# Kernel tuning notes

Hardware: AMD Instinct MI355X
Metric: run time of the kernel (lower is better)

## Reference

```python
import jax, jax.numpy as jnp
import numpy as np

N = 8192          # total proposals
D_IN = 256 * 7 * 7  # 12544
HID = 1024
C = 3


def setup_inputs() -> dict:
    key = jax.random.key(0)
    ks = jax.random.split(key, 9)
    s_in = 1.0 / np.sqrt(D_IN)
    s_h = 1.0 / np.sqrt(HID)
    return {
        "feature_vectors": jax.random.normal(ks[0], (N, D_IN), dtype=jnp.float32),
        "W1": jax.random.uniform(ks[1], (D_IN, HID), jnp.float32, -s_in, s_in),
        "b1": jax.random.uniform(ks[2], (HID,), jnp.float32, -s_in, s_in),
        "W2": jax.random.uniform(ks[3], (HID, HID), jnp.float32, -s_h, s_h),
        "b2": jax.random.uniform(ks[4], (HID,), jnp.float32, -s_h, s_h),
        "Wc": jax.random.uniform(ks[5], (HID, C + 1), jnp.float32, -s_h, s_h),
        "bc": jax.random.uniform(ks[6], (C + 1,), jnp.float32, -s_h, s_h),
        "Wr": jax.random.uniform(ks[7], (HID, 4 * C), jnp.float32, -s_h, s_h),
        "br": jax.random.uniform(ks[8], (4 * C,), jnp.float32, -s_h, s_h),
    }


def reference(feature_vectors, W1, b1, W2, b2, Wc, bc, Wr, br):
    # intermediate: Linear -> Linear -> ReLU (note: no ReLU between the two Linears,
    # matching the original nn.Sequential ordering)
    h = feature_vectors @ W1 + b1          # [N, 1024]
    h = h @ W2 + b2                        # [N, 1024]
    h = jax.nn.relu(h)
    class_logits = jax.nn.softmax(h @ Wc + bc, axis=-1)  # [N, C+1]
    box_pred = h @ Wr + br                  # [N, 4C]
    return class_logits, box_pred
```

## Files before the change

### kernel.cpp

```cpp
#include <hip/hip_runtime.h>
#include <hip/hip_bf16.h>
#include <stdint.h>

using u16 = unsigned short;
using u32 = unsigned int;

typedef __attribute__((ext_vector_type(8))) short short8;
typedef __attribute__((ext_vector_type(4))) float floatx4;

__device__ __forceinline__ u16 f2bf(float f) {
  __hip_bfloat16 h = __float2bfloat16(f);
  return *reinterpret_cast<u16*>(&h);
}

__device__ __forceinline__ void gl_lds16(const void* g, void* l) {
  __builtin_amdgcn_global_load_lds((const __attribute__((address_space(1))) void*)g,
                                   (__attribute__((address_space(3))) void*)l, 16, 0, 0);
}

__global__ __launch_bounds__(256)
void transpose_to_bf16(const float* __restrict__ in, u16* __restrict__ out,
                       int R, int Cc) {
  __shared__ float tile[32][33];
  int c0 = blockIdx.x * 32;
  int r0 = blockIdx.y * 32;
  int tx = threadIdx.x;
  int ty = threadIdx.y;
#pragma unroll
  for (int i = 0; i < 32; i += 8)
    tile[ty + i][tx] = in[(size_t)(r0 + ty + i) * Cc + c0 + tx];
  __syncthreads();
#pragma unroll
  for (int i = 0; i < 32; i += 8)
    out[(size_t)(c0 + ty + i) * R + r0 + tx] = f2bf(tile[tx][ty + i]);
}

#define MM(i, j, va, vb) \
  acc[i][j] = __builtin_amdgcn_mfma_f32_16x16x32_bf16(va, vb, acc[i][j], 0, 0, 0)
#define MEMF() asm volatile("" ::: "memory")
#define BAR() do { MEMF(); __builtin_amdgcn_s_barrier(); MEMF(); } while (0)

constexpr int A_BUF  = 256 * 64;
constexpr int B_BUF  = 128 * 64;
constexpr int B_BASE = 3 * A_BUF;
constexpr int LDS_BYTES = (3 * A_BUF + 3 * B_BUF) * 2;

#define STAGE_AH(h, bufo) \
  do { gl_lds16(apt[h][0], lds + (bufo) + adst[h][0]); apt[h][0] += 64; \
       gl_lds16(apt[h][1], lds + (bufo) + adst[h][1]); apt[h][1] += 64; } while (0)
#define STAGE_BH(h, bufo) \
  do { gl_lds16(bpt[h], lds + (bufo) + bdst[h]); bpt[h] += 64; } while (0)

template <bool RELU>
__global__ __launch_bounds__(512, 2)
void gemm256(const u16* __restrict__ A, const u16* __restrict__ BT,
             const float* __restrict__ bias, u16* __restrict__ C,
             int N, int K) {
  extern __shared__ u16 lds[];
  const int tid  = threadIdx.x;
  const int lane = tid & 63;
  const int wave = tid >> 6;
  const int wm = wave >> 1;
  const int wn = wave & 1;
  const int row = lane & 15;
  const int kq  = lane >> 4;
  const int sw  = lane & 7;

  const int orig = blockIdx.y * 8 + blockIdx.x;
  const int rr = ((orig & 7) << 5) | (orig >> 3);
  const int n0 = (rr & 7) * 128;
  const int m0 = (rr >> 3) * 256;

  const int o0 = ((kq) ^ sw) * 8;
  const int o1 = ((4 | kq) ^ sw) * 8;
  const int ar0 = (wm * 64 + row) * 64;
  const int ar1 = ar0 + 16 * 64;
  const int ar2 = ar0 + 32 * 64;
  const int ar3 = ar0 + 48 * 64;
  const int br0 = (wn * 64 + row) * 64;
  const int br1 = br0 + 16 * 64;
  const int br2 = br0 + 32 * 64;
  const int br3 = br0 + 48 * 64;

  const u16* apt[2][2];
  int adst[2][2];
#pragma unroll
  for (int h = 0; h < 2; ++h)
#pragma unroll
    for (int L = 0; L < 2; ++L) {
      int i = L * 512 + tid;
      int rg = h * 128 + (i >> 3);
      int c = i & 7;
      apt[h][L] = A + (size_t)(m0 + rg) * K + ((c ^ (rg & 7)) * 8);
      adst[h][L] = h * 8192 + L * 4096 + wave * 512;
    }
  const u16* bpt[2];
  int bdst[2];
#pragma unroll
  for (int h = 0; h < 2; ++h) {
    int rg = h * 64 + (tid >> 3);
    int c = tid & 7;
    bpt[h] = BT + (size_t)(n0 + rg) * K + ((c ^ (rg & 7)) * 8);
    bdst[h] = B_BASE + h * 4096 + wave * 512;
  }

  STAGE_AH(0, 0);      STAGE_AH(1, 0);      STAGE_BH(0, 0);     STAGE_BH(1, 0);
  STAGE_AH(0, A_BUF);  STAGE_AH(1, A_BUF);  STAGE_BH(0, B_BUF); STAGE_BH(1, B_BUF);
  asm volatile("s_waitcnt vmcnt(6)" ::: "memory");
  BAR();

  floatx4 acc[4][4] = {};
  int cb = 0, sb = 2;
  const int NT = K >> 6;
  for (int T = 0; T < NT; ++T) {
    const bool st = (T + 2 < NT);
    const u16* Ac = lds + cb * A_BUF;
    const u16* Bc = lds + B_BASE + cb * B_BUF;
    const int sA = sb * A_BUF;
    const int sB = sb * B_BUF;

    short8 a0k0, a0k1, a1k0, a1k1, a2k0, a2k1, a3k0, a3k1;
    short8 b0k0, b0k1, b1k0, b1k1, b2k0, b2k1, b3k0, b3k1;

    a0k0 = *(const short8*)(Ac + ar0 + o0);
    a0k1 = *(const short8*)(Ac + ar0 + o1);
    a1k0 = *(const short8*)(Ac + ar1 + o0);
    a1k1 = *(const short8*)(Ac + ar1 + o1);
    b0k0 = *(const short8*)(Bc + br0 + o0);
    b0k1 = *(const short8*)(Bc + br0 + o1);
    b1k0 = *(const short8*)(Bc + br1 + o0);
    b1k1 = *(const short8*)(Bc + br1 + o1);
    if (st) STAGE_AH(0, sA);
    BAR();
    __builtin_amdgcn_s_setprio(1);
    MM(0, 0, a0k0, b0k0); MM(0, 1, a0k0, b1k0);
    MM(1, 0, a1k0, b0k0); MM(1, 1, a1k0, b1k0);
    MM(0, 0, a0k1, b0k1); MM(0, 1, a0k1, b1k1);
    MM(1, 0, a1k1, b0k1); MM(1, 1, a1k1, b1k1);
    __builtin_amdgcn_s_setprio(0);
    BAR();

    b2k0 = *(const short8*)(Bc + br2 + o0);
    b2k1 = *(const short8*)(Bc + br2 + o1);
    b3k0 = *(const short8*)(Bc + br3 + o0);
    b3k1 = *(const short8*)(Bc + br3 + o1);
    if (st) STAGE_AH(1, sA);
    BAR();
    __builtin_amdgcn_s_setprio(1);
    MM(0, 2, a0k0, b2k0); MM(0, 3, a0k0, b3k0);
    MM(1, 2, a1k0, b2k0); MM(1, 3, a1k0, b3k0);
    MM(0, 2, a0k1, b2k1); MM(0, 3, a0k1, b3k1);
    MM(1, 2, a1k1, b2k1); MM(1, 3, a1k1, b3k1);
    __builtin_amdgcn_s_setprio(0);
    BAR();

    a2k0 = *(const short8*)(Ac + ar2 + o0);
    a2k1 = *(const short8*)(Ac + ar2 + o1);
    a3k0 = *(const short8*)(Ac + ar3 + o0);
    a3k1 = *(const short8*)(Ac + ar3 + o1);
    if (st) STAGE_BH(0, sB);
    BAR();
    __builtin_amdgcn_s_setprio(1);
    MM(2, 2, a2k0, b2k0); MM(2, 3, a2k0, b3k0);
    MM(3, 2, a3k0, b2k0); MM(3, 3, a3k0, b3k0);
    MM(2, 2, a2k1, b2k1); MM(2, 3, a2k1, b3k1);
    MM(3, 2, a3k1, b2k1); MM(3, 3, a3k1, b3k1);
    __builtin_amdgcn_s_setprio(0);
    BAR();

    if (st) STAGE_BH(1, sB);
    BAR();
    __builtin_amdgcn_s_setprio(1);
    MM(2, 0, a2k0, b0k0); MM(2, 1, a2k0, b1k0);
    MM(3, 0, a3k0, b0k0); MM(3, 1, a3k0, b1k0);
    MM(2, 0, a2k1, b0k1); MM(2, 1, a2k1, b1k1);
    MM(3, 0, a3k1, b0k1); MM(3, 1, a3k1, b1k1);
    __builtin_amdgcn_s_setprio(0);
    if (st) asm volatile("s_waitcnt vmcnt(6)" ::: "memory");
    else    asm volatile("s_waitcnt vmcnt(0)" ::: "memory");
    BAR();

    cb = (cb == 2) ? 0 : cb + 1;
    sb = (sb == 2) ? 0 : sb + 1;
  }

#pragma unroll
  for (int mt = 0; mt < 4; ++mt) {
#pragma unroll
    for (int nt = 0; nt < 4; ++nt) {
      int gm = m0 + wm * 64 + mt * 16 + kq * 4;
      int gn = n0 + wn * 64 + nt * 16 + row;
      float bv = bias[gn];
#pragma unroll
      for (int r = 0; r < 4; ++r) {
        float v = acc[mt][nt][r] + bv;
        if (RELU) v = fmaxf(v, 0.f);
        C[(size_t)(gm + r) * N + gn] = f2bf(v);
      }
    }
  }
}

constexpr int FA_BUF  = 256 * 64;
constexpr int FB_BUF  = 128 * 64;
constexpr int FB_BASE = 2 * FA_BUF;
constexpr int LDS_BYTES_F = (2 * FA_BUF + 2 * FB_BUF) * 2;

__device__ __forceinline__ void cvtw64(u16* dst, float4 v) {
  u32 lo = (u32)f2bf(v.x) | ((u32)f2bf(v.y) << 16);
  u32 hi = (u32)f2bf(v.z) | ((u32)f2bf(v.w) << 16);
  *(uint2*)dst = make_uint2(lo, hi);
}

__global__ __launch_bounds__(512, 2)
void gemm256F(const float* __restrict__ A, const u16* __restrict__ BT,
              const float* __restrict__ bias, u16* __restrict__ C,
              int N, int K) {
  extern __shared__ u16 lds[];
  const int tid  = threadIdx.x;
  const int lane = tid & 63;
  const int wave = tid >> 6;
  const int wm = wave >> 1;
  const int wn = wave & 1;
  const int row = lane & 15;
  const int kq  = lane >> 4;
  const int sw  = lane & 7;

  const int orig = blockIdx.y * 8 + blockIdx.x;
  const int rr = ((orig & 7) << 5) | (orig >> 3);
  const int n0 = (rr & 7) * 128;
  const int m0 = (rr >> 3) * 256;

  const int o0 = ((kq) ^ sw) * 8;
  const int o1 = ((4 | kq) ^ sw) * 8;
  const int ar0 = (wm * 64 + row) * 64;
  const int ar1 = ar0 + 16 * 64;
  const int ar2 = ar0 + 32 * 64;
  const int ar3 = ar0 + 48 * 64;
  const int br0 = (wn * 64 + row) * 64;
  const int br1 = br0 + 16 * 64;
  const int br2 = br0 + 32 * 64;
  const int br3 = br0 + 48 * 64;

  const u16* bpt[2];
  int bdst[2];
#pragma unroll
  for (int h = 0; h < 2; ++h) {
    int rg = h * 64 + (tid >> 3);
    int c = tid & 7;
    bpt[h] = BT + (size_t)(n0 + rg) * K + ((c ^ (rg & 7)) * 8);
    bdst[h] = h * 4096 + wave * 512;
  }

  const float* aFk = A + (size_t)(m0 + (tid >> 4)) * K + (tid & 15) * 4;
  const int r0t = tid >> 4;
  const int c4 = tid & 15;
  const int adst0 = r0t * 64 + (((c4 >> 1) ^ (r0t & 7)) * 8) + (c4 & 1) * 4;

  float4 rA[2][4];

#define FSTAGE_ISSUE(nB_)                                              \
  do {                                                                 \
    MEMF();                                                            \
    gl_lds16(bpt[0], lds + (nB_) + bdst[0]); bpt[0] += 64;             \
    gl_lds16(bpt[1], lds + (nB_) + bdst[1]); bpt[1] += 64;             \
    MEMF();                                                            \
    _Pragma("unroll")                                                  \
    for (int h = 0; h < 2; ++h)                                        \
      _Pragma("unroll")                                                \
      for (int i = 0; i < 4; ++i)                                      \
        rA[h][i] = *(const float4*)(aFk + (size_t)(h * 128 + i * 32) * K); \
    aFk += 64;                                                         \
    MEMF();                                                            \
  } while (0)

#define FSTAGE_WRITE(nA_)                                              \
  do {                                                                 \
    asm volatile("s_waitcnt vmcnt(4)" ::: "memory");                   \
    _Pragma("unroll")                                                  \
    for (int i = 0; i < 4; ++i)                                        \
      cvtw64(lds + (nA_) + adst0 + (i * 32) * 64, rA[0][i]);           \
    asm volatile("s_waitcnt vmcnt(0)" ::: "memory");                   \
    _Pragma("unroll")                                                  \
    for (int i = 0; i < 4; ++i)                                        \
      cvtw64(lds + (nA_) + adst0 + ((128 + i * 32)) * 64, rA[1][i]);   \
  } while (0)

  FSTAGE_ISSUE(FB_BASE + 0);
  FSTAGE_WRITE(0);
  asm volatile("s_waitcnt lgkmcnt(0)" ::: "memory");
  BAR();

  floatx4 acc[4][4] = {};
  const int NT = K >> 6;
  for (int T = 0; T < NT; ++T) {
    const int cur = T & 1;
    const bool st = (T + 1 < NT);
    const u16* Ac = lds + cur * FA_BUF;
    const u16* Bc = lds + FB_BASE + cur * FB_BUF;
    const int nA = (cur ^ 1) * FA_BUF;
    const int nB = FB_BASE + (cur ^ 1) * FB_BUF;

    short8 a0k0, a0k1, a1k0, a1k1, a2k0, a2k1, a3k0, a3k1;
    short8 b0k0, b0k1, b1k0, b1k1, b2k0, b2k1, b3k0, b3k1;

    a0k0 = *(const short8*)(Ac + ar0 + o0);
    a0k1 = *(const short8*)(Ac + ar0 + o1);
    a1k0 = *(const short8*)(Ac + ar1 + o0);
    a1k1 = *(const short8*)(Ac + ar1 + o1);
    b0k0 = *(const short8*)(Bc + br0 + o0);
    b0k1 = *(const short8*)(Bc + br0 + o1);
    b1k0 = *(const short8*)(Bc + br1 + o0);
    b1k1 = *(const short8*)(Bc + br1 + o1);
    if (st) FSTAGE_ISSUE(nB);
    BAR();
    __builtin_amdgcn_s_setprio(1);
    MM(0, 0, a0k0, b0k0); MM(0, 1, a0k0, b1k0);
    MM(1, 0, a1k0, b0k0); MM(1, 1, a1k0, b1k0);
    MM(0, 0, a0k1, b0k1); MM(0, 1, a0k1, b1k1);
    MM(1, 0, a1k1, b0k1); MM(1, 1, a1k1, b1k1);
    __builtin_amdgcn_s_setprio(0);
    BAR();

    b2k0 = *(const short8*)(Bc + br2 + o0);
    b2k1 = *(const short8*)(Bc + br2 + o1);
    b3k0 = *(const short8*)(Bc + br3 + o0);
    b3k1 = *(const short8*)(Bc + br3 + o1);
    BAR();
    __builtin_amdgcn_s_setprio(1);
    MM(0, 2, a0k0, b2k0); MM(0, 3, a0k0, b3k0);
    MM(1, 2, a1k0, b2k0); MM(1, 3, a1k0, b3k0);
    MM(0, 2, a0k1, b2k1); MM(0, 3, a0k1, b3k1);
    MM(1, 2, a1k1, b2k1); MM(1, 3, a1k1, b3k1);
    __builtin_amdgcn_s_setprio(0);
    BAR();

    a2k0 = *(const short8*)(Ac + ar2 + o0);
    a2k1 = *(const short8*)(Ac + ar2 + o1);
    a3k0 = *(const short8*)(Ac + ar3 + o0);
    a3k1 = *(const short8*)(Ac + ar3 + o1);
    BAR();
    __builtin_amdgcn_s_setprio(1);
    MM(2, 2, a2k0, b2k0); MM(2, 3, a2k0, b3k0);
    MM(3, 2, a3k0, b2k0); MM(3, 3, a3k0, b3k0);
    MM(2, 2, a2k1, b2k1); MM(2, 3, a2k1, b3k1);
    MM(3, 2, a3k1, b2k1); MM(3, 3, a3k1, b3k1);
    __builtin_amdgcn_s_setprio(0);
    BAR();

    if (st) FSTAGE_WRITE(nA);
    __builtin_amdgcn_s_setprio(1);
    MM(2, 0, a2k0, b0k0); MM(2, 1, a2k0, b1k0);
    MM(3, 0, a3k0, b0k0); MM(3, 1, a3k0, b1k0);
    MM(2, 0, a2k1, b0k1); MM(2, 1, a2k1, b1k1);
    MM(3, 0, a3k1, b0k1); MM(3, 1, a3k1, b1k1);
    __builtin_amdgcn_s_setprio(0);
    asm volatile("s_waitcnt lgkmcnt(0)" ::: "memory");
    BAR();
  }

#pragma unroll
  for (int mt = 0; mt < 4; ++mt) {
#pragma unroll
    for (int nt = 0; nt < 4; ++nt) {
      int gm = m0 + wm * 64 + mt * 16 + kq * 4;
      int gn = n0 + wn * 64 + nt * 16 + row;
      float bv = bias[gn];
#pragma unroll
      for (int r = 0; r < 4; ++r) {
        float v = acc[mt][nt][r] + bv;
        C[(size_t)(gm + r) * N + gn] = f2bf(v);
      }
    }
  }
#undef FSTAGE_ISSUE
#undef FSTAGE_WRITE
}

__device__ __forceinline__ float wave_sum(float v) {
#pragma unroll
  for (int m = 32; m >= 1; m >>= 1) v += __shfl_xor(v, m, 64);
  return v;
}

__global__ __launch_bounds__(256)
void head_kernel(const u16* __restrict__ H, const float* __restrict__ Wc,
                 const float* __restrict__ bc, const float* __restrict__ Wr,
                 const float* __restrict__ br, float* __restrict__ out) {
  const int rowi = blockIdx.x * 4 + (threadIdx.x >> 6);
  const int lane = threadIdx.x & 63;
  const u16* h = H + (size_t)rowi * 1024 + lane * 16;
  uint4 p0 = *(const uint4*)h;
  uint4 p1 = *(const uint4*)(h + 8);
  u32 w[8] = {p0.x, p0.y, p0.z, p0.w, p1.x, p1.y, p1.z, p1.w};
  float x[16];
#pragma unroll
  for (int i = 0; i < 8; ++i) {
    union { u32 u; float f; } lo, hi;
    lo.u = w[i] << 16;
    hi.u = w[i] & 0xffff0000u;
    x[2 * i] = lo.f;
    x[2 * i + 1] = hi.f;
  }
  float ac[4] = {};
  float ar[12] = {};
  const int kbase = lane * 16;
#pragma unroll
  for (int j = 0; j < 16; ++j) {
    float xv = x[j];
    const float* wc = Wc + (size_t)(kbase + j) * 4;
#pragma unroll
    for (int c = 0; c < 4; ++c) ac[c] = fmaf(xv, wc[c], ac[c]);
    const float* wr = Wr + (size_t)(kbase + j) * 12;
#pragma unroll
    for (int r = 0; r < 12; ++r) ar[r] = fmaf(xv, wr[r], ar[r]);
  }
#pragma unroll
  for (int c = 0; c < 4; ++c) ac[c] = wave_sum(ac[c]);
#pragma unroll
  for (int r = 0; r < 12; ++r) ar[r] = wave_sum(ar[r]);

  if (lane == 0) {
    float lg[4], mx = -1e30f;
#pragma unroll
    for (int c = 0; c < 4; ++c) { lg[c] = ac[c] + bc[c]; mx = fmaxf(mx, lg[c]); }
    float s = 0.f;
#pragma unroll
    for (int c = 0; c < 4; ++c) { lg[c] = __expf(lg[c] - mx); s += lg[c]; }
    float inv = 1.f / s;
#pragma unroll
    for (int c = 0; c < 4; ++c) out[(size_t)rowi * 4 + c] = lg[c] * inv;
    float* ob = out + 8192 * 4;
#pragma unroll
    for (int r = 0; r < 12; ++r) ob[(size_t)rowi * 12 + r] = ar[r] + br[r];
  }
}

extern "C" void kernel_launch(void* const* d_in, const int* in_sizes, int n_in,
                              void* d_out, int out_size, void* d_ws, size_t ws_size,
                              hipStream_t stream) {
  const float* X  = (const float*)d_in[0];
  const float* W1 = (const float*)d_in[1];
  const float* b1 = (const float*)d_in[2];
  const float* W2 = (const float*)d_in[3];
  const float* b2 = (const float*)d_in[4];
  const float* Wc = (const float*)d_in[5];
  const float* bc = (const float*)d_in[6];
  const float* Wr = (const float*)d_in[7];
  const float* br = (const float*)d_in[8];

  constexpr int NP = 8192, DIN = 12544, HID = 1024;
  char* ws = (char*)d_ws;
  u16* W1T = (u16*)ws;
  u16* W2T = (u16*)(ws + (size_t)HID * DIN * 2);
  u16* H1  = (u16*)((char*)W2T + (size_t)HID * HID * 2);
  u16* Hb  = H1 + (size_t)NP * HID;
  (void)ws_size;

  static bool s_attr = false;
  if (!s_attr) {
    hipFuncSetAttribute(reinterpret_cast<const void*>(gemm256F),
                        hipFuncAttributeMaxDynamicSharedMemorySize, LDS_BYTES_F);
    hipFuncSetAttribute(reinterpret_cast<const void*>(gemm256<true>),
                        hipFuncAttributeMaxDynamicSharedMemorySize, LDS_BYTES);
    s_attr = true;
  }

  transpose_to_bf16<<<dim3(HID / 32, DIN / 32), dim3(32, 8), 0, stream>>>(W1, W1T, DIN, HID);
  transpose_to_bf16<<<dim3(HID / 32, HID / 32), dim3(32, 8), 0, stream>>>(W2, W2T, HID, HID);

  gemm256F<<<dim3(8, NP / 256), 512, LDS_BYTES_F, stream>>>(
      X, W1T, b1, H1, HID, DIN);
  gemm256<true><<<dim3(8, NP / 256), 512, LDS_BYTES, stream>>>(
      H1, W2T, b2, Hb, HID, HID);
  head_kernel<<<NP / 4, 256, 0, stream>>>(Hb, Wc, bc, Wr, br, (float*)d_out);
}
```

Baseline: 1.070 ms.

## Deepen fp32-A GEMM pipeline to three LDS stages with two-tile register prefetch

Restructures the first GEMM (fp32 features converted to bf16 in-kernel) from a double-buffered LDS pipeline to a triple-buffered one. B tiles are issued two iterations ahead, and A global loads go into alternating register sets, so each A tile gets about a full iteration of latency before it is converted and written to LDS. The loop is unrolled by two so the register sets swap statically, and the kernel now reuses the shared LDS_BYTES layout. This raises register pressure (16 float4 held for A) and LDS use, which may reduce occupancy under launch_bounds(512,2).

After: 1.025 ms. -4.2%, faster.

```diff
diff --git a/kernel.cpp b/kernel.cpp
--- a/kernel.cpp
+++ b/kernel.cpp
@@ -201,11 +201,6 @@
   }
 }
 
-constexpr int FA_BUF  = 256 * 64;
-constexpr int FB_BUF  = 128 * 64;
-constexpr int FB_BASE = 2 * FA_BUF;
-constexpr int LDS_BYTES_F = (2 * FA_BUF + 2 * FB_BUF) * 2;
-
 __device__ __forceinline__ void cvtw64(u16* dst, float4 v) {
   u32 lo = (u32)f2bf(v.x) | ((u32)f2bf(v.y) << 16);
   u32 hi = (u32)f2bf(v.z) | ((u32)f2bf(v.w) << 16);
@@ -257,107 +252,121 @@
   const int c4 = tid & 15;
   const int adst0 = r0t * 64 + (((c4 >> 1) ^ (r0t & 7)) * 8) + (c4 & 1) * 4;
 
-  float4 rA[2][4];
-
-#define FSTAGE_ISSUE(nB_)                                              \
-  do {                                                                 \
-    MEMF();                                                            \
-    gl_lds16(bpt[0], lds + (nB_) + bdst[0]); bpt[0] += 64;             \
-    gl_lds16(bpt[1], lds + (nB_) + bdst[1]); bpt[1] += 64;             \
-    MEMF();                                                            \
-    _Pragma("unroll")                                                  \
-    for (int h = 0; h < 2; ++h)                                        \
-      _Pragma("unroll")                                                \
-      for (int i = 0; i < 4; ++i)                                      \
-        rA[h][i] = *(const float4*)(aFk + (size_t)(h * 128 + i * 32) * K); \
-    aFk += 64;                                                         \
-    MEMF();                                                            \
-  } while (0)
-
-#define FSTAGE_WRITE(nA_)                                              \
-  do {                                                                 \
-    asm volatile("s_waitcnt vmcnt(4)" ::: "memory");                   \
-    _Pragma("unroll")                                                  \
-    for (int i = 0; i < 4; ++i)                                        \
-      cvtw64(lds + (nA_) + adst0 + (i * 32) * 64, rA[0][i]);           \
-    asm volatile("s_waitcnt vmcnt(0)" ::: "memory");                   \
-    _Pragma("unroll")                                                  \
-    for (int i = 0; i < 4; ++i)                                        \
-      cvtw64(lds + (nA_) + adst0 + ((128 + i * 32)) * 64, rA[1][i]);   \
-  } while (0)
-
-  FSTAGE_ISSUE(FB_BASE + 0);
-  FSTAGE_WRITE(0);
+  float4 rA0[8], rA1[8];
+
+  MEMF();
+  gl_lds16(bpt[0], lds + B_BASE + bdst[0]); bpt[0] += 64;
+  gl_lds16(bpt[1], lds + B_BASE + bdst[1]); bpt[1] += 64;
+#pragma unroll
+  for (int i = 0; i < 8; ++i)
+    rA0[i] = *(const float4*)(aFk + (size_t)(i * 32) * K);
+  aFk += 64;
+  gl_lds16(bpt[0], lds + B_BASE + B_BUF + bdst[0]); bpt[0] += 64;
+  gl_lds16(bpt[1], lds + B_BASE + B_BUF + bdst[1]); bpt[1] += 64;
+#pragma unroll
+  for (int i = 0; i < 8; ++i)
+    rA1[i] = *(const float4*)(aFk + (size_t)(i * 32) * K);
+  aFk += 64;
+  MEMF();
+  asm volatile("s_waitcnt vmcnt(10)" ::: "memory");
+#pragma unroll
+  for (int i = 0; i < 8; ++i)
+    cvtw64(lds + adst0 + (i * 32) * 64, rA0[i]);
   asm volatile("s_waitcnt lgkmcnt(0)" ::: "memory");
   BAR();
 
   floatx4 acc[4][4] = {};
+  int cb = 0, sb = 2, anb = 1;
   const int NT = K >> 6;
-  for (int T = 0; T < NT; ++T) {
-    const int cur = T & 1;
-    const bool st = (T + 1 < NT);
-    const u16* Ac = lds + cur * FA_BUF;
-    const u16* Bc = lds + FB_BASE + cur * FB_BUF;
-    const int nA = (cur ^ 1) * FA_BUF;
-    const int nB = FB_BASE + (cur ^ 1) * FB_BUF;
-
-    short8 a0k0, a0k1, a1k0, a1k1, a2k0, a2k1, a3k0, a3k1;
-    short8 b0k0, b0k1, b1k0, b1k1, b2k0, b2k1, b3k0, b3k1;
-
-    a0k0 = *(const short8*)(Ac + ar0 + o0);
-    a0k1 = *(const short8*)(Ac + ar0 + o1);
-    a1k0 = *(const short8*)(Ac + ar1 + o0);
-    a1k1 = *(const short8*)(Ac + ar1 + o1);
-    b0k0 = *(const short8*)(Bc + br0 + o0);
-    b0k1 = *(const short8*)(Bc + br0 + o1);
-    b1k0 = *(const short8*)(Bc + br1 + o0);
-    b1k1 = *(const short8*)(Bc + br1 + o1);
-    if (st) FSTAGE_ISSUE(nB);
-    BAR();
-    __builtin_amdgcn_s_setprio(1);
-    MM(0, 0, a0k0, b0k0); MM(0, 1, a0k0, b1k0);
-    MM(1, 0, a1k0, b0k0); MM(1, 1, a1k0, b1k0);
-    MM(0, 0, a0k1, b0k1); MM(0, 1, a0k1, b1k1);
-    MM(1, 0, a1k1, b0k1); MM(1, 1, a1k1, b1k1);
-    __builtin_amdgcn_s_setprio(0);
-    BAR();
-
-    b2k0 = *(const short8*)(Bc + br2 + o0);
-    b2k1 = *(const short8*)(Bc + br2 + o1);
-    b3k0 = *(const short8*)(Bc + br3 + o0);
-    b3k1 = *(const short8*)(Bc + br3 + o1);
-    BAR();
-    __builtin_amdgcn_s_setprio(1);
-    MM(0, 2, a0k0, b2k0); MM(0, 3, a0k0, b3k0);
-    MM(1, 2, a1k0, b2k0); MM(1, 3, a1k0, b3k0);
-    MM(0, 2, a0k1, b2k1); MM(0, 3, a0k1, b3k1);
-    MM(1, 2, a1k1, b2k1); MM(1, 3, a1k1, b3k1);
-    __builtin_amdgcn_s_setprio(0);
-    BAR();
-
-    a2k0 = *(const short8*)(Ac + ar2 + o0);
-    a2k1 = *(const short8*)(Ac + ar2 + o1);
-    a3k0 = *(const short8*)(Ac + ar3 + o0);
-    a3k1 = *(const short8*)(Ac + ar3 + o1);
-    BAR();
-    __builtin_amdgcn_s_setprio(1);
-    MM(2, 2, a2k0, b2k0); MM(2, 3, a2k0, b3k0);
-    MM(3, 2, a3k0, b2k0); MM(3, 3, a3k0, b3k0);
-    MM(2, 2, a2k1, b2k1); MM(2, 3, a2k1, b3k1);
-    MM(3, 2, a3k1, b2k1); MM(3, 3, a3k1, b3k1);
-    __builtin_amdgcn_s_setprio(0);
-    BAR();
-
-    if (st) FSTAGE_WRITE(nA);
-    __builtin_amdgcn_s_setprio(1);
-    MM(2, 0, a2k0, b0k0); MM(2, 1, a2k0, b1k0);
-    MM(3, 0, a3k0, b0k0); MM(3, 1, a3k0, b1k0);
-    MM(2, 0, a2k1, b0k1); MM(2, 1, a2k1, b1k1);
-    MM(3, 0, a3k1, b0k1); MM(3, 1, a3k1, b1k1);
-    __builtin_amdgcn_s_setprio(0);
-    asm volatile("s_waitcnt lgkmcnt(0)" ::: "memory");
-    BAR();
-  }
+
+#define FTILE(T_, RSI, RSW)                                                \
+  do {                                                                     \
+    const bool st2 = (T_) + 2 < NT;                                        \
+    const bool st1 = (T_) + 1 < NT;                                        \
+    const u16* Ac = lds + cb * A_BUF;                                      \
+    const u16* Bc = lds + B_BASE + cb * B_BUF;                             \
+    short8 a0k0, a0k1, a1k0, a1k1, a2k0, a2k1, a3k0, a3k1;                 \
+    short8 b0k0, b0k1, b1k0, b1k1, b2k0, b2k1, b3k0, b3k1;                 \
+           \
+    a0k0 = *(const short8*)(Ac + ar0 + o0);                                \
+    a0k1 = *(const short8*)(Ac + ar0 + o1);                                \
+    a1k0 = *(const short8*)(Ac + ar1 + o0);                                \
+    a1k1 = *(const short8*)(Ac + ar1 + o1);                                \
+    b0k0 = *(const short8*)(Bc + br0 + o0);                                \
+    b0k1 = *(const short8*)(Bc + br0 + o1);                                \
+    b1k0 = *(const short8*)(Bc + br1 + o0);                                \
+    b1k1 = *(const short8*)(Bc + br1 + o1);                                \
+    if (st2) {                                                             \
+      MEMF();                                                              \
+      gl_lds16(bpt[0], lds + B_BASE + sb * B_BUF + bdst[0]); bpt[0] += 64; \
+      gl_lds16(bpt[1], lds + B_BASE + sb * B_BUF + bdst[1]); bpt[1] += 64; \
+      _Pragma("unroll")                                                    \
+      for (int i = 0; i < 8; ++i)                                          \
+        RSI[i] = *(const float4*)(aFk + (size_t)(i * 32) * K);             \
+      aFk += 64;                                                           \
+      MEMF();                                                              \
+    }                                                                      \
+    BAR();                                                                 \
+    __builtin_amdgcn_s_setprio(1);                                         \
+    MM(0, 0, a0k0, b0k0); MM(0, 1, a0k0, b1k0);                            \
+    MM(1, 0, a1k0, b0k0); MM(1, 1, a1k0, b1k0);                            \
+    MM(0, 0, a0k1, b0k1); MM(0, 1, a0k1, b1k1);                            \
+    MM(1, 0, a1k1, b0k1); MM(1, 1, a1k1, b1k1);                            \
+    __builtin_amdgcn_s_setprio(0);                                         \
+    BAR();                                                                 \
+                                                                   \
+    b2k0 = *(const short8*)(Bc + br2 + o0);                                \
+    b2k1 = *(const short8*)(Bc + br2 + o1);                                \
+    b3k0 = *(const short8*)(Bc + br3 + o0);                                \
+    b3k1 = *(const short8*)(Bc + br3 + o1);                                \
+    BAR();                                                                 \
+    __builtin_amdgcn_s_setprio(1);                                         \
+    MM(0, 2, a0k0, b2k0); MM(0, 3, a0k0, b3k0);                            \
+    MM(1, 2, a1k0, b2k0); MM(1, 3, a1k0, b3k0);                            \
+    MM(0, 2, a0k1, b2k1); MM(0, 3, a0k1, b3k1);                            \
+    MM(1, 2, a1k1, b2k1); MM(1, 3, a1k1, b3k1);                            \
+    __builtin_amdgcn_s_setprio(0);                                         \
+    BAR();                                                                 \
+                                                                   \
+    a2k0 = *(const short8*)(Ac + ar2 + o0);                                \
+    a2k1 = *(const short8*)(Ac + ar2 + o1);                                \
+    a3k0 = *(const short8*)(Ac + ar3 + o0);                                \
+    a3k1 = *(const short8*)(Ac + ar3 + o1);                                \
+    BAR();                                                                 \
+    __builtin_amdgcn_s_setprio(1);                                         \
+    MM(2, 2, a2k0, b2k0); MM(2, 3, a2k0, b3k0);                            \
+    MM(3, 2, a3k0, b2k0); MM(3, 3, a3k0, b3k0);                            \
+    MM(2, 2, a2k1, b2k1); MM(2, 3, a2k1, b3k1);                            \
+    MM(3, 2, a3k1, b2k1); MM(3, 3, a3k1, b3k1);                            \
+    __builtin_amdgcn_s_setprio(0);                                         \
+    BAR();                                                                 \
+             \
+    if (st1) {                                                             \
+      if (st2) asm volatile("s_waitcnt vmcnt(10)" ::: "memory");           \
+      else     asm volatile("s_waitcnt vmcnt(0)" ::: "memory");            \
+      u16* Aw = lds + anb * A_BUF;                                         \
+      _Pragma("unroll")                                                    \
+      for (int i = 0; i < 8; ++i)                                          \
+        cvtw64(Aw + adst0 + (i * 32) * 64, RSW[i]);                        \
+    }                                                                      \
+    __builtin_amdgcn_s_setprio(1);                                         \
+    MM(2, 0, a2k0, b0k0); MM(2, 1, a2k0, b1k0);                            \
+    MM(3, 0, a3k0, b0k0); MM(3, 1, a3k0, b1k0);                            \
+    MM(2, 0, a2k1, b0k1); MM(2, 1, a2k1, b1k1);                            \
+    MM(3, 0, a3k1, b0k1); MM(3, 1, a3k1, b1k1);                            \
+    __builtin_amdgcn_s_setprio(0);                                         \
+    asm volatile("s_waitcnt lgkmcnt(0)" ::: "memory");                     \
+    BAR();                                                                 \
+    cb = (cb == 2) ? 0 : cb + 1;                                           \
+    sb = (sb == 2) ? 0 : sb + 1;                                           \
+    anb = (anb == 2) ? 0 : anb + 1;                                        \
+  } while (0)
+
+  for (int T = 0; T < NT; T += 2) {
+    FTILE(T, rA0, rA1);
+    FTILE(T + 1, rA1, rA0);
+  }
+#undef FTILE
 
 #pragma unroll
   for (int mt = 0; mt < 4; ++mt) {
@@ -373,8 +382,6 @@
       }
     }
   }
-#undef FSTAGE_ISSUE
-#undef FSTAGE_WRITE
 }
 
 __device__ __forceinline__ float wave_sum(float v) {
@@ -460,7 +467,7 @@
   static bool s_attr = false;
   if (!s_attr) {
     hipFuncSetAttribute(reinterpret_cast<const void*>(gemm256F),
-                        hipFuncAttributeMaxDynamicSharedMemorySize, LDS_BYTES_F);
+                        hipFuncAttributeMaxDynamicSharedMemorySize, LDS_BYTES);
     hipFuncSetAttribute(reinterpret_cast<const void*>(gemm256<true>),
                         hipFuncAttributeMaxDynamicSharedMemorySize, LDS_BYTES);
     s_attr = true;
@@ -469,7 +476,7 @@
   transpose_to_bf16<<<dim3(HID / 32, DIN / 32), dim3(32, 8), 0, stream>>>(W1, W1T, DIN, HID);
   transpose_to_bf16<<<dim3(HID / 32, HID / 32), dim3(32, 8), 0, stream>>>(W2, W2T, HID, HID);
 
-  gemm256F<<<dim3(8, NP / 256), 512, LDS_BYTES_F, stream>>>(
+  gemm256F<<<dim3(8, NP / 256), 512, LDS_BYTES, stream>>>(
       X, W1T, b1, H1, HID, DIN);
   gemm256<true><<<dim3(8, NP / 256), 512, LDS_BYTES, stream>>>(
       H1, W2T, b2, Hb, HID, HID);
```
